# Optimization experiments

Measured on AMD Instinct MI355X. Metric: run time of the kernel, lower is better.

Reference implementation:

```python
import jax, jax.numpy as jnp
import numpy as np

B, S, D, H = 2, 2048, 1024, 16
DK = D // H


def setup_inputs() -> dict:
    key = jax.random.key(0)
    ks = jax.random.split(key, 11)
    s = 1.0 / np.sqrt(D)
    inp = {
        "q": jax.random.normal(ks[0], (B, S, D), jnp.float32),
        "k": jax.random.normal(ks[1], (B, S, D), jnp.float32),
        "v": jax.random.normal(ks[2], (B, S, D), jnp.float32),
        "mask": jnp.tril(jnp.ones((S, S), jnp.int32))[None, None],  # causal [1,1,S,S]
        "w_q": jax.random.normal(ks[3], (D, D), jnp.float32) * s,
        "b_q": jax.random.normal(ks[4], (D,), jnp.float32) * 0.01,
        "w_k": jax.random.normal(ks[5], (D, D), jnp.float32) * s,
        "b_k": jax.random.normal(ks[6], (D,), jnp.float32) * 0.01,
        "w_v": jax.random.normal(ks[7], (D, D), jnp.float32) * s,
        "b_v": jax.random.normal(ks[8], (D,), jnp.float32) * 0.01,
        "w_o": jax.random.normal(ks[9], (D, D), jnp.float32) * s,
        "b_o": jax.random.normal(ks[10], (D,), jnp.float32) * 0.01,
    }
    return inp


def reference(q, k, v, mask, w_q, b_q, w_k, b_k, w_v, b_v, w_o, b_o):
    # Linear projections (torch Linear: x @ W.T + b)
    query = q @ w_q.T + b_q  # [B,S,D]
    key_ = k @ w_k.T + b_k
    value = v @ w_v.T + b_v
    # split heads -> [B,H,S,DK]
    def split(x):
        return x.reshape(B, S, H, DK).transpose(0, 2, 1, 3)
    qh, kh, vh = split(query), split(key_), split(value)
    scores = jnp.einsum("bhqd,bhkd->bhqk", qh, kh) / jnp.sqrt(jnp.float32(DK))
    scores = jnp.where(mask == 0, jnp.float32(-1e9), scores)
    attn = jax.nn.softmax(scores, axis=-1)
    out = jnp.einsum("bhqk,bhkd->bhqd", attn, vh)  # [B,H,S,DK]
    out = out.transpose(0, 2, 1, 3).reshape(B, S, D)
    return out @ w_o.T + b_o
```

## Files before the change

kernel.cpp:

```cpp
#include <hip/hip_runtime.h>


typedef __attribute__((ext_vector_type(8))) short bf16x8;
typedef __attribute__((ext_vector_type(4))) float floatx4;
typedef __attribute__((ext_vector_type(4))) unsigned short u16x4;

#define S_LEN 2048
#define D_MODEL 1024
#define N_HEADS 16
#define D_HEAD 64
#define M_ROWS 4096
#define QSCALE 0.18033688011112042f

__device__ __forceinline__ unsigned short f32_to_bf16(float f) {
  unsigned int u = __builtin_bit_cast(unsigned int, f);
  u += 0x7FFFu + ((u >> 16) & 1u);
  return (unsigned short)(u >> 16);
}

__global__ __launch_bounds__(256) void cvt_w(
    const float* __restrict__ w0, const float* __restrict__ w1,
    const float* __restrict__ w2, const float* __restrict__ w3,
    unsigned short* __restrict__ dst) {
  const int z = blockIdx.y;
  const float* src = (z == 0) ? w0 : (z == 1) ? w1 : (z == 2) ? w2 : w3;
  unsigned short* d = dst + ((long)z << 20);
  const int n4 = 1 << 18;
  for (int i = blockIdx.x * 256 + threadIdx.x; i < n4; i += gridDim.x * 256) {
    float4 f = ((const float4*)src)[i];
    u16x4 o;
    o[0] = f32_to_bf16(f.x); o[1] = f32_to_bf16(f.y);
    o[2] = f32_to_bf16(f.z); o[3] = f32_to_bf16(f.w);
    ((u16x4*)d)[i] = o;
  }
}

__global__ __launch_bounds__(256) void cvt_x(
    const float* __restrict__ x0, const float* __restrict__ x1,
    const float* __restrict__ x2, unsigned short* __restrict__ dst) {
  const int z = blockIdx.y;
  const float* src = (z == 0) ? x0 : (z == 1) ? x1 : x2;
  unsigned short* d = dst + (long)z * M_ROWS * D_MODEL;
  const int n4 = (M_ROWS * D_MODEL) / 4;
  for (int i = blockIdx.x * 256 + threadIdx.x; i < n4; i += gridDim.x * 256) {
    float4 f = ((const float4*)src)[i];
    u16x4 o;
    o[0] = f32_to_bf16(f.x); o[1] = f32_to_bf16(f.y);
    o[2] = f32_to_bf16(f.z); o[3] = f32_to_bf16(f.w);
    ((u16x4*)d)[i] = o;
  }
}

#define GK 1024
#define GN 1024
#define LDP 72

template <bool XPRE>
__global__ __launch_bounds__(256, 3) void qkv_gemm(
    const float* __restrict__ Xq, const float* __restrict__ Xk, const float* __restrict__ Xv,
    const unsigned short* __restrict__ Xb,
    const unsigned short* __restrict__ Wb,
    const float* __restrict__ bq, const float* __restrict__ bk, const float* __restrict__ bv,
    unsigned short* __restrict__ Yq, unsigned short* __restrict__ Yk,
    unsigned short* __restrict__ Yvt) {
  __shared__ __align__(16) unsigned short As[128 * LDP];
  __shared__ __align__(16) unsigned short Bs[128 * LDP];

  const int z = blockIdx.z;
  const unsigned short* W = Wb + ((long)z << 20);
  const float* bias = (z == 0) ? bq : ((z == 1) ? bk : bv);

  const int r0 = blockIdx.x * 128;
  const int n0 = blockIdx.y * 128;
  const int tid = threadIdx.x;
  const int lane = tid & 63;
  const int wave = tid >> 6;
  const int quad = lane >> 4;
  const int ln = lane & 15;
  const int wm = (wave >> 1) * 64;
  const int wn = (wave & 1) * 64;

  floatx4 acc[4][4];
#pragma unroll
  for (int i = 0; i < 4; i++)
#pragma unroll
    for (int j = 0; j < 4; j++) acc[i][j] = (floatx4){0.f, 0.f, 0.f, 0.f};

  const int srow = tid >> 1;
  const int scol = (tid & 1) * 32;
  unsigned short* Asw = As + srow * LDP + scol;
  unsigned short* Bsw = Bs + srow * LDP + scol;
  const unsigned short* Bp = W + (long)(n0 + srow) * GK + scol;
  const float* ApF = nullptr;
  const unsigned short* ApH = nullptr;
  if constexpr (XPRE) {
    ApH = Xb + (long)z * M_ROWS * D_MODEL + (long)(r0 + srow) * GK + scol;
  } else {
    const float* X = (z == 0) ? Xq : ((z == 1) ? Xk : Xv);
    ApF = X + (long)(r0 + srow) * GK + scol;
  }

  for (int k0 = 0; k0 < GK; k0 += 64) {
    float4 b0 = *(const float4*)(Bp + k0);
    float4 b1 = *(const float4*)(Bp + k0 + 8);
    float4 b2 = *(const float4*)(Bp + k0 + 16);
    float4 b3 = *(const float4*)(Bp + k0 + 24);
    float4 a0, a1, a2, a3;
    if constexpr (XPRE) {
      a0 = *(const float4*)(ApH + k0);
      a1 = *(const float4*)(ApH + k0 + 8);
      a2 = *(const float4*)(ApH + k0 + 16);
      a3 = *(const float4*)(ApH + k0 + 24);
    } else {
      unsigned short ua[32] __attribute__((aligned(16)));
      float fa[32] __attribute__((aligned(16)));
#pragma unroll
      for (int c = 0; c < 8; c++)
        *(float4*)(fa + c * 4) = *(const float4*)(ApF + k0 + c * 4);
#pragma unroll
      for (int j = 0; j < 32; j++) ua[j] = f32_to_bf16(fa[j]);
      a0 = *(float4*)(ua); a1 = *(float4*)(ua + 8);
      a2 = *(float4*)(ua + 16); a3 = *(float4*)(ua + 24);
    }
    __syncthreads();
    *(float4*)(Asw) = a0;      *(float4*)(Asw + 8) = a1;
    *(float4*)(Asw + 16) = a2; *(float4*)(Asw + 24) = a3;
    *(float4*)(Bsw) = b0;      *(float4*)(Bsw + 8) = b1;
    *(float4*)(Bsw + 16) = b2; *(float4*)(Bsw + 24) = b3;
    __syncthreads();

#pragma unroll
    for (int ks = 0; ks < 64; ks += 32) {
      bf16x8 af[4], bfr[4];
#pragma unroll
      for (int mt = 0; mt < 4; mt++)
        af[mt] = *(const bf16x8*)(As + (wm + mt * 16 + ln) * LDP + ks + quad * 8);
#pragma unroll
      for (int nt = 0; nt < 4; nt++)
        bfr[nt] = *(const bf16x8*)(Bs + (wn + nt * 16 + ln) * LDP + ks + quad * 8);
#pragma unroll
      for (int mt = 0; mt < 4; mt++)
#pragma unroll
        for (int nt = 0; nt < 4; nt++)
          acc[mt][nt] = __builtin_amdgcn_mfma_f32_16x16x32_bf16(af[mt], bfr[nt], acc[mt][nt], 0, 0, 0);
    }
  }

#pragma unroll
  for (int nt = 0; nt < 4; nt++) {
    const int n = n0 + wn + nt * 16 + ln;
    const float bv = bias[n];
#pragma unroll
    for (int mt = 0; mt < 4; mt++) {
      const int r = r0 + wm + mt * 16 + quad * 4;
      if (z == 2) {
        u16x4 pk;
#pragma unroll
        for (int reg = 0; reg < 4; reg++) pk[reg] = f32_to_bf16(acc[mt][nt][reg] + bv);
        *(u16x4*)(Yvt + (long)n * M_ROWS + r) = pk;
      } else if (z == 0) {
#pragma unroll
        for (int reg = 0; reg < 4; reg++)
          Yq[(long)(r + reg) * GN + n] = f32_to_bf16((acc[mt][nt][reg] + bv) * QSCALE);
      } else {
#pragma unroll
        for (int reg = 0; reg < 4; reg++)
          Yk[(long)(r + reg) * GN + n] = f32_to_bf16(acc[mt][nt][reg] + bv);
      }
    }
  }
}

__global__ __launch_bounds__(256, 3) void out_gemm(
    const unsigned short* __restrict__ X,
    const unsigned short* __restrict__ W,
    const float* __restrict__ bias,
    float* __restrict__ Y) {
  __shared__ __align__(16) unsigned short As[64 * LDP];
  __shared__ __align__(16) unsigned short Bs[128 * LDP];

  const int r0 = blockIdx.x * 64;
  const int n0 = blockIdx.y * 128;
  const int tid = threadIdx.x;
  const int lane = tid & 63;
  const int wave = tid >> 6;
  const int quad = lane >> 4;
  const int ln = lane & 15;
  const int wm = (wave >> 1) * 32;
  const int wn = (wave & 1) * 64;

  floatx4 acc[2][4];
#pragma unroll
  for (int i = 0; i < 2; i++)
#pragma unroll
    for (int j = 0; j < 4; j++) acc[i][j] = (floatx4){0.f, 0.f, 0.f, 0.f};

  const int arow = tid >> 2;
  const int acol = (tid & 3) * 16;
  const unsigned short* Ap = X + (long)(r0 + arow) * GK + acol;
  unsigned short* Asw = As + arow * LDP + acol;
  const int brow = tid >> 1;
  const int bcol = (tid & 1) * 32;
  const unsigned short* Bp = W + (long)(n0 + brow) * GK + bcol;
  unsigned short* Bsw = Bs + brow * LDP + bcol;

  for (int k0 = 0; k0 < GK; k0 += 64) {
    float4 a0 = *(const float4*)(Ap + k0);
    float4 a1 = *(const float4*)(Ap + k0 + 8);
    float4 b0 = *(const float4*)(Bp + k0);
    float4 b1 = *(const float4*)(Bp + k0 + 8);
    float4 b2 = *(const float4*)(Bp + k0 + 16);
    float4 b3 = *(const float4*)(Bp + k0 + 24);
    __syncthreads();
    *(float4*)(Asw) = a0;      *(float4*)(Asw + 8) = a1;
    *(float4*)(Bsw) = b0;      *(float4*)(Bsw + 8) = b1;
    *(float4*)(Bsw + 16) = b2; *(float4*)(Bsw + 24) = b3;
    __syncthreads();

#pragma unroll
    for (int ks = 0; ks < 64; ks += 32) {
      bf16x8 af[2], bfr[4];
#pragma unroll
      for (int mt = 0; mt < 2; mt++)
        af[mt] = *(const bf16x8*)(As + (wm + mt * 16 + ln) * LDP + ks + quad * 8);
#pragma unroll
      for (int nt = 0; nt < 4; nt++)
        bfr[nt] = *(const bf16x8*)(Bs + (wn + nt * 16 + ln) * LDP + ks + quad * 8);
#pragma unroll
      for (int mt = 0; mt < 2; mt++)
#pragma unroll
        for (int nt = 0; nt < 4; nt++)
          acc[mt][nt] = __builtin_amdgcn_mfma_f32_16x16x32_bf16(af[mt], bfr[nt], acc[mt][nt], 0, 0, 0);
    }
  }

#pragma unroll
  for (int nt = 0; nt < 4; nt++) {
    const int n = n0 + wn + nt * 16 + ln;
    const float bv = bias[n];
#pragma unroll
    for (int mt = 0; mt < 2; mt++) {
      const int r = r0 + wm + mt * 16 + quad * 4;
#pragma unroll
      for (int reg = 0; reg < 4; reg++)
        Y[(long)(r + reg) * GN + n] = acc[mt][nt][reg] + bv;
    }
  }
}

#define PSTR 72

__global__ __launch_bounds__(64, 2) void attn_causal(
    const unsigned short* __restrict__ Q,
    const unsigned short* __restrict__ K,
    const unsigned short* __restrict__ Vt,
    unsigned short* __restrict__ O) {
  __shared__ __align__(16) unsigned short PbA[16 * PSTR];
  __shared__ __align__(16) unsigned short PbB[16 * PSTR];

  const int bh = blockIdx.x;
  const int pr = blockIdx.y;
  const int b = bh >> 4;
  const int h = bh & 15;

  const int lane = threadIdx.x;
  const int quad = lane >> 4;
  const int ln = lane & 15;

  const int s1 = pr, s2 = 127 - pr;
  const int q0A = s1 * 16, q0B = s2 * 16;
  const int nkt1 = (s1 >> 2) + 1;
  const int nkt2 = (s2 >> 2) + 1;

  const unsigned short* Qb = Q + (long)b * S_LEN * D_MODEL + h * D_HEAD;
  const unsigned short* Kb = K + (long)b * S_LEN * D_MODEL + h * D_HEAD;
  const unsigned short* Vb = Vt + (long)h * D_HEAD * M_ROWS + b * S_LEN;

  bf16x8 qfA[2], qfB[2];
  qfA[0] = *(const bf16x8*)(Qb + (long)(q0A + ln) * D_MODEL + quad * 8);
  qfA[1] = *(const bf16x8*)(Qb + (long)(q0A + ln) * D_MODEL + 32 + quad * 8);
  qfB[0] = *(const bf16x8*)(Qb + (long)(q0B + ln) * D_MODEL + quad * 8);
  qfB[1] = *(const bf16x8*)(Qb + (long)(q0B + ln) * D_MODEL + 32 + quad * 8);

  float mA = -1e30f, lA = 0.f, mB = -1e30f, lB = 0.f;
  floatx4 oA[4], oB[4];
#pragma unroll
  for (int nt = 0; nt < 4; nt++) {
    oA[nt] = (floatx4){0.f, 0.f, 0.f, 0.f};
    oB[nt] = (floatx4){0.f, 0.f, 0.f, 0.f};
  }

  auto loadKV = [&](bf16x8 (&kf)[4][2], bf16x8 (&vf)[4][2], int kt) {
    const int kv0 = kt * 64;
#pragma unroll
    for (int ct = 0; ct < 4; ct++) {
      const unsigned short* kp = Kb + (long)(kv0 + ct * 16 + ln) * D_MODEL + quad * 8;
      kf[ct][0] = *(const bf16x8*)(kp);
      kf[ct][1] = *(const bf16x8*)(kp + 32);
      const unsigned short* vp = Vb + (long)(ct * 16 + ln) * M_ROWS + kv0 + quad * 8;
      vf[ct][0] = *(const bf16x8*)(vp);
      vf[ct][1] = *(const bf16x8*)(vp + 32);
    }
  };

  auto iter = [&](bf16x8 (&kf)[4][2], bf16x8 (&vf)[4][2], int kt) {
    const int kv0 = kt * 64;
    const bool aAct = (kt < nkt1);

    floatx4 sB[4], sA[4];
#pragma unroll
    for (int ct = 0; ct < 4; ct++) {
      sB[ct] = (floatx4){0.f, 0.f, 0.f, 0.f};
      sB[ct] = __builtin_amdgcn_mfma_f32_16x16x32_bf16(kf[ct][0], qfB[0], sB[ct], 0, 0, 0);
      sB[ct] = __builtin_amdgcn_mfma_f32_16x16x32_bf16(kf[ct][1], qfB[1], sB[ct], 0, 0, 0);
    }
    if (aAct) {
#pragma unroll
      for (int ct = 0; ct < 4; ct++) {
        sA[ct] = (floatx4){0.f, 0.f, 0.f, 0.f};
        sA[ct] = __builtin_amdgcn_mfma_f32_16x16x32_bf16(kf[ct][0], qfA[0], sA[ct], 0, 0, 0);
        sA[ct] = __builtin_amdgcn_mfma_f32_16x16x32_bf16(kf[ct][1], qfA[1], sA[ct], 0, 0, 0);
      }
    }

    {
      float tmax = -1e30f;
      if (kt == nkt2 - 1) {
        const int qg = q0B + ln;
#pragma unroll
        for (int ct = 0; ct < 4; ct++) {
          const int kvb = kv0 + ct * 16 + quad * 4;
#pragma unroll
          for (int reg = 0; reg < 4; reg++) {
            float sv = sB[ct][reg];
            if (kvb + reg > qg) sv = -1e30f;
            sB[ct][reg] = sv;
            tmax = fmaxf(tmax, sv);
          }
        }
      } else {
#pragma unroll
        for (int ct = 0; ct < 4; ct++)
#pragma unroll
          for (int reg = 0; reg < 4; reg++) tmax = fmaxf(tmax, sB[ct][reg]);
      }
      tmax = fmaxf(tmax, __shfl_xor(tmax, 16, 64));
      tmax = fmaxf(tmax, __shfl_xor(tmax, 32, 64));
      const float mnew = fmaxf(mB, tmax);
      const float alpha = exp2f(mB - mnew);
      mB = mnew;
      float rsum = 0.f;
#pragma unroll
      for (int ct = 0; ct < 4; ct++) {
        u16x4 pk;
#pragma unroll
        for (int reg = 0; reg < 4; reg++) {
          const float p = exp2f(sB[ct][reg] - mB);
          rsum += p;
          pk[reg] = f32_to_bf16(p);
        }
        *(u16x4*)(PbB + ln * PSTR + ct * 16 + quad * 4) = pk;
      }
      rsum += __shfl_xor(rsum, 16, 64);
      rsum += __shfl_xor(rsum, 32, 64);
      lB = lB * alpha + rsum;
#pragma unroll
      for (int nt = 0; nt < 4; nt++)
#pragma unroll
        for (int reg = 0; reg < 4; reg++) oB[nt][reg] *= alpha;
    }

    if (aAct) {
      float tmax = -1e30f;
      if (kt == nkt1 - 1) {
        const int qg = q0A + ln;
#pragma unroll
        for (int ct = 0; ct < 4; ct++) {
          const int kvb = kv0 + ct * 16 + quad * 4;
#pragma unroll
          for (int reg = 0; reg < 4; reg++) {
            float sv = sA[ct][reg];
            if (kvb + reg > qg) sv = -1e30f;
            sA[ct][reg] = sv;
            tmax = fmaxf(tmax, sv);
          }
        }
      } else {
#pragma unroll
        for (int ct = 0; ct < 4; ct++)
#pragma unroll
          for (int reg = 0; reg < 4; reg++) tmax = fmaxf(tmax, sA[ct][reg]);
      }
      tmax = fmaxf(tmax, __shfl_xor(tmax, 16, 64));
      tmax = fmaxf(tmax, __shfl_xor(tmax, 32, 64));
      const float mnew = fmaxf(mA, tmax);
      const float alpha = exp2f(mA - mnew);
      mA = mnew;
      float rsum = 0.f;
#pragma unroll
      for (int ct = 0; ct < 4; ct++) {
        u16x4 pk;
#pragma unroll
        for (int reg = 0; reg < 4; reg++) {
          const float p = exp2f(sA[ct][reg] - mA);
          rsum += p;
          pk[reg] = f32_to_bf16(p);
        }
        *(u16x4*)(PbA + ln * PSTR + ct * 16 + quad * 4) = pk;
      }
      rsum += __shfl_xor(rsum, 16, 64);
      rsum += __shfl_xor(rsum, 32, 64);
      lA = lA * alpha + rsum;
#pragma unroll
      for (int nt = 0; nt < 4; nt++)
#pragma unroll
        for (int reg = 0; reg < 4; reg++) oA[nt][reg] *= alpha;
    }

    __builtin_amdgcn_wave_barrier();

    {
      bf16x8 p0 = *(const bf16x8*)(PbB + ln * PSTR + quad * 8);
      bf16x8 p1 = *(const bf16x8*)(PbB + ln * PSTR + 32 + quad * 8);
#pragma unroll
      for (int nt = 0; nt < 4; nt++) {
        oB[nt] = __builtin_amdgcn_mfma_f32_16x16x32_bf16(vf[nt][0], p0, oB[nt], 0, 0, 0);
        oB[nt] = __builtin_amdgcn_mfma_f32_16x16x32_bf16(vf[nt][1], p1, oB[nt], 0, 0, 0);
      }
    }
    if (aAct) {
      bf16x8 p0 = *(const bf16x8*)(PbA + ln * PSTR + quad * 8);
      bf16x8 p1 = *(const bf16x8*)(PbA + ln * PSTR + 32 + quad * 8);
#pragma unroll
      for (int nt = 0; nt < 4; nt++) {
        oA[nt] = __builtin_amdgcn_mfma_f32_16x16x32_bf16(vf[nt][0], p0, oA[nt], 0, 0, 0);
        oA[nt] = __builtin_amdgcn_mfma_f32_16x16x32_bf16(vf[nt][1], p1, oA[nt], 0, 0, 0);
      }
    }
    __builtin_amdgcn_wave_barrier();
  };

  bf16x8 kf0[4][2], vf0[4][2], kf1[4][2], vf1[4][2];
  loadKV(kf0, vf0, 0);
#pragma unroll 1
  for (int kt = 0; kt < nkt2; kt += 2) {
    if (kt + 1 < nkt2) loadKV(kf1, vf1, kt + 1);
    iter(kf0, vf0, kt);
    if (kt + 1 >= nkt2) break;
    if (kt + 2 < nkt2) loadKV(kf0, vf0, kt + 2);
    iter(kf1, vf1, kt + 1);
  }

  {
    const float inv = 1.0f / lA;
    unsigned short* op = O + (long)b * S_LEN * D_MODEL + (long)(q0A + ln) * D_MODEL + h * D_HEAD;
#pragma unroll
    for (int nt = 0; nt < 4; nt++) {
      u16x4 pk;
#pragma unroll
      for (int reg = 0; reg < 4; reg++) pk[reg] = f32_to_bf16(oA[nt][reg] * inv);
      *(u16x4*)(op + nt * 16 + quad * 4) = pk;
    }
  }
  {
    const float inv = 1.0f / lB;
    unsigned short* op = O + (long)b * S_LEN * D_MODEL + (long)(q0B + ln) * D_MODEL + h * D_HEAD;
#pragma unroll
    for (int nt = 0; nt < 4; nt++) {
      u16x4 pk;
#pragma unroll
      for (int reg = 0; reg < 4; reg++) pk[reg] = f32_to_bf16(oB[nt][reg] * inv);
      *(u16x4*)(op + nt * 16 + quad * 4) = pk;
    }
  }
}

extern "C" void kernel_launch(void* const* d_in, const int* in_sizes, int n_in,
                              void* d_out, int out_size, void* d_ws, size_t ws_size,
                              hipStream_t stream) {
  const float* q = (const float*)d_in[0];
  const float* k = (const float*)d_in[1];
  const float* v = (const float*)d_in[2];
  const float* w_q = (const float*)d_in[4];
  const float* b_q = (const float*)d_in[5];
  const float* w_k = (const float*)d_in[6];
  const float* b_k = (const float*)d_in[7];
  const float* w_v = (const float*)d_in[8];
  const float* b_v = (const float*)d_in[9];
  const float* w_o = (const float*)d_in[10];
  const float* b_o = (const float*)d_in[11];
  float* out = (float*)d_out;

  unsigned short* ws = (unsigned short*)d_ws;
  const long NE = (long)M_ROWS * D_MODEL;
  const bool xpre = (ws_size >= (size_t)7 * NE * sizeof(unsigned short));

  unsigned short *Qp, *Kp, *Vpt, *AO, *Wb, *Xb;
  if (xpre) {
    Qp = ws;
    Kp = ws + NE;
    Vpt = ws + 2 * NE;
    Wb = ws + 3 * NE;
    Xb = ws + 4 * NE;
    AO = ws + 4 * NE;
  } else {
    Qp = ws;
    Kp = ws + NE;
    Vpt = ws + 2 * NE;
    AO = ws + 3 * NE;
    Wb = ws + 4 * NE;
    Xb = nullptr;
  }

  cvt_w<<<dim3(256, 4), 256, 0, stream>>>(w_q, w_k, w_v, w_o, Wb);
  if (xpre) {
    cvt_x<<<dim3(512, 3), 256, 0, stream>>>(q, k, v, Xb);
    qkv_gemm<true><<<dim3(M_ROWS / 128, GN / 128, 3), 256, 0, stream>>>(
        q, k, v, Xb, Wb, b_q, b_k, b_v, Qp, Kp, Vpt);
  } else {
    qkv_gemm<false><<<dim3(M_ROWS / 128, GN / 128, 3), 256, 0, stream>>>(
        q, k, v, nullptr, Wb, b_q, b_k, b_v, Qp, Kp, Vpt);
  }
  attn_causal<<<dim3(2 * N_HEADS, 64), 64, 0, stream>>>(Qp, Kp, Vpt, AO);
  out_gemm<<<dim3(M_ROWS / 64, GN / 128), 256, 0, stream>>>(AO, Wb + 3 * (1 << 20), b_o, out);
}
```

Before: 283.1 us.

## Use async global-to-LDS loads in GEMMs, fuse X conversion, drop online softmax max

Drops the separate fp32-to-bf16 activation conversion kernel, so the QKV GEMM converts X in registers. B tiles (and both operands in the output GEMM) now go straight from global memory into unpadded LDS through global_load_lds. The attention kernel stops tracking a running max and rescaling, exponentiates raw scores directly, and gets row sums from extra MFMAs against a ones vector. Removing the max subtraction risks exp overflow for large scores, and the unpadded LDS layout may bring bank conflicts.

```diff
diff --git a/kernel.cpp b/kernel.cpp
--- a/kernel.cpp
+++ b/kernel.cpp
@@ -16,6 +16,12 @@
   unsigned int u = __builtin_bit_cast(unsigned int, f);
   u += 0x7FFFu + ((u >> 16) & 1u);
   return (unsigned short)(u >> 16);
+}
+
+__device__ __forceinline__ void async16(const void* g, void* l) {
+  __builtin_amdgcn_global_load_lds(
+      (const __attribute__((address_space(1))) unsigned int*)g,
+      (__attribute__((address_space(3))) unsigned int*)l, 16, 0, 0);
 }
 
 __global__ __launch_bounds__(256) void cvt_w(
@@ -35,38 +41,21 @@
   }
 }
 
-__global__ __launch_bounds__(256) void cvt_x(
-    const float* __restrict__ x0, const float* __restrict__ x1,
-    const float* __restrict__ x2, unsigned short* __restrict__ dst) {
-  const int z = blockIdx.y;
-  const float* src = (z == 0) ? x0 : (z == 1) ? x1 : x2;
-  unsigned short* d = dst + (long)z * M_ROWS * D_MODEL;
-  const int n4 = (M_ROWS * D_MODEL) / 4;
-  for (int i = blockIdx.x * 256 + threadIdx.x; i < n4; i += gridDim.x * 256) {
-    float4 f = ((const float4*)src)[i];
-    u16x4 o;
-    o[0] = f32_to_bf16(f.x); o[1] = f32_to_bf16(f.y);
-    o[2] = f32_to_bf16(f.z); o[3] = f32_to_bf16(f.w);
-    ((u16x4*)d)[i] = o;
-  }
-}
-
 #define GK 1024
 #define GN 1024
-#define LDP 72
-
-template <bool XPRE>
+#define BK 64
+
 __global__ __launch_bounds__(256, 3) void qkv_gemm(
     const float* __restrict__ Xq, const float* __restrict__ Xk, const float* __restrict__ Xv,
-    const unsigned short* __restrict__ Xb,
     const unsigned short* __restrict__ Wb,
     const float* __restrict__ bq, const float* __restrict__ bk, const float* __restrict__ bv,
     unsigned short* __restrict__ Yq, unsigned short* __restrict__ Yk,
     unsigned short* __restrict__ Yvt) {
-  __shared__ __align__(16) unsigned short As[128 * LDP];
-  __shared__ __align__(16) unsigned short Bs[128 * LDP];
+  __shared__ __align__(16) unsigned short As[128 * BK];
+  __shared__ __align__(16) unsigned short Bs[128 * BK];
 
   const int z = blockIdx.z;
+  const float* X = (z == 0) ? Xq : ((z == 1) ? Xk : Xv);
   const unsigned short* W = Wb + ((long)z << 20);
   const float* bias = (z == 0) ? bq : ((z == 1) ? bk : bv);
 
@@ -86,58 +75,43 @@
 #pragma unroll
     for (int j = 0; j < 4; j++) acc[i][j] = (floatx4){0.f, 0.f, 0.f, 0.f};
 
-  const int srow = tid >> 1;
-  const int scol = (tid & 1) * 32;
-  unsigned short* Asw = As + srow * LDP + scol;
-  unsigned short* Bsw = Bs + srow * LDP + scol;
-  const unsigned short* Bp = W + (long)(n0 + srow) * GK + scol;
-  const float* ApF = nullptr;
-  const unsigned short* ApH = nullptr;
-  if constexpr (XPRE) {
-    ApH = Xb + (long)z * M_ROWS * D_MODEL + (long)(r0 + srow) * GK + scol;
-  } else {
-    const float* X = (z == 0) ? Xq : ((z == 1) ? Xk : Xv);
-    ApF = X + (long)(r0 + srow) * GK + scol;
-  }
-
-  for (int k0 = 0; k0 < GK; k0 += 64) {
-    float4 b0 = *(const float4*)(Bp + k0);
-    float4 b1 = *(const float4*)(Bp + k0 + 8);
-    float4 b2 = *(const float4*)(Bp + k0 + 16);
-    float4 b3 = *(const float4*)(Bp + k0 + 24);
-    float4 a0, a1, a2, a3;
-    if constexpr (XPRE) {
-      a0 = *(const float4*)(ApH + k0);
-      a1 = *(const float4*)(ApH + k0 + 8);
-      a2 = *(const float4*)(ApH + k0 + 16);
-      a3 = *(const float4*)(ApH + k0 + 24);
-    } else {
-      unsigned short ua[32] __attribute__((aligned(16)));
-      float fa[32] __attribute__((aligned(16)));
-#pragma unroll
-      for (int c = 0; c < 8; c++)
-        *(float4*)(fa + c * 4) = *(const float4*)(ApF + k0 + c * 4);
-#pragma unroll
-      for (int j = 0; j < 32; j++) ua[j] = f32_to_bf16(fa[j]);
-      a0 = *(float4*)(ua); a1 = *(float4*)(ua + 8);
-      a2 = *(float4*)(ua + 16); a3 = *(float4*)(ua + 24);
-    }
+  const int arow = tid >> 3;
+  const int acol = (tid & 7) * 8;
+  const float* Ap = X + (long)(r0 + arow) * GK + acol;
+  unsigned short* Asw = As + tid * 8;
+  const int brow = lane >> 3;
+  const int bcol = (lane & 7) * 8;
+  const unsigned short* Bp = W + (long)(n0 + brow) * GK + bcol;
+
+  for (int k0 = 0; k0 < GK; k0 += BK) {
+    float fa[32] __attribute__((aligned(16)));
+#pragma unroll
+    for (int c = 0; c < 4; c++) {
+      *(float4*)(fa + c * 8)     = *(const float4*)(Ap + (long)c * 32 * GK + k0);
+      *(float4*)(fa + c * 8 + 4) = *(const float4*)(Ap + (long)c * 32 * GK + k0 + 4);
+    }
+    unsigned short ua[32] __attribute__((aligned(16)));
+#pragma unroll
+    for (int j = 0; j < 32; j++) ua[j] = f32_to_bf16(fa[j]);
+
     __syncthreads();
-    *(float4*)(Asw) = a0;      *(float4*)(Asw + 8) = a1;
-    *(float4*)(Asw + 16) = a2; *(float4*)(Asw + 24) = a3;
-    *(float4*)(Bsw) = b0;      *(float4*)(Bsw + 8) = b1;
-    *(float4*)(Bsw + 16) = b2; *(float4*)(Bsw + 24) = b3;
+#pragma unroll
+    for (int j = 0; j < 4; j++)
+      async16(Bp + (long)(wave * 4 + j) * 8 * GK + k0, Bs + (wave * 4 + j) * 512);
+#pragma unroll
+    for (int c = 0; c < 4; c++)
+      *(float4*)(Asw + c * 2048) = *(float4*)(ua + c * 8);
     __syncthreads();
 
 #pragma unroll
-    for (int ks = 0; ks < 64; ks += 32) {
+    for (int ks = 0; ks < BK; ks += 32) {
       bf16x8 af[4], bfr[4];
 #pragma unroll
       for (int mt = 0; mt < 4; mt++)
-        af[mt] = *(const bf16x8*)(As + (wm + mt * 16 + ln) * LDP + ks + quad * 8);
+        af[mt] = *(const bf16x8*)(As + (wm + mt * 16 + ln) * BK + ks + quad * 8);
 #pragma unroll
       for (int nt = 0; nt < 4; nt++)
-        bfr[nt] = *(const bf16x8*)(Bs + (wn + nt * 16 + ln) * LDP + ks + quad * 8);
+        bfr[nt] = *(const bf16x8*)(Bs + (wn + nt * 16 + ln) * BK + ks + quad * 8);
 #pragma unroll
       for (int mt = 0; mt < 4; mt++)
 #pragma unroll
@@ -176,8 +150,8 @@
     const unsigned short* __restrict__ W,
     const float* __restrict__ bias,
     float* __restrict__ Y) {
-  __shared__ __align__(16) unsigned short As[64 * LDP];
-  __shared__ __align__(16) unsigned short Bs[128 * LDP];
+  __shared__ __align__(16) unsigned short As[64 * BK];
+  __shared__ __align__(16) unsigned short Bs[128 * BK];
 
   const int r0 = blockIdx.x * 64;
   const int n0 = blockIdx.y * 128;
@@ -195,37 +169,30 @@
 #pragma unroll
     for (int j = 0; j < 4; j++) acc[i][j] = (floatx4){0.f, 0.f, 0.f, 0.f};
 
-  const int arow = tid >> 2;
-  const int acol = (tid & 3) * 16;
-  const unsigned short* Ap = X + (long)(r0 + arow) * GK + acol;
-  unsigned short* Asw = As + arow * LDP + acol;
-  const int brow = tid >> 1;
-  const int bcol = (tid & 1) * 32;
-  const unsigned short* Bp = W + (long)(n0 + brow) * GK + bcol;
-  unsigned short* Bsw = Bs + brow * LDP + bcol;
-
-  for (int k0 = 0; k0 < GK; k0 += 64) {
-    float4 a0 = *(const float4*)(Ap + k0);
-    float4 a1 = *(const float4*)(Ap + k0 + 8);
-    float4 b0 = *(const float4*)(Bp + k0);
-    float4 b1 = *(const float4*)(Bp + k0 + 8);
-    float4 b2 = *(const float4*)(Bp + k0 + 16);
-    float4 b3 = *(const float4*)(Bp + k0 + 24);
+  const int srow = lane >> 3;
+  const int scol = (lane & 7) * 8;
+  const unsigned short* Apb = X + (long)(r0 + srow) * GK + scol;
+  const unsigned short* Bpb = W + (long)(n0 + srow) * GK + scol;
+
+  for (int k0 = 0; k0 < GK; k0 += BK) {
     __syncthreads();
-    *(float4*)(Asw) = a0;      *(float4*)(Asw + 8) = a1;
-    *(float4*)(Bsw) = b0;      *(float4*)(Bsw + 8) = b1;
-    *(float4*)(Bsw + 16) = b2; *(float4*)(Bsw + 24) = b3;
+#pragma unroll
+    for (int j = 0; j < 2; j++)
+      async16(Apb + (long)(wave * 2 + j) * 8 * GK + k0, As + (wave * 2 + j) * 512);
+#pragma unroll
+    for (int j = 0; j < 4; j++)
+      async16(Bpb + (long)(wave * 4 + j) * 8 * GK + k0, Bs + (wave * 4 + j) * 512);
     __syncthreads();
 
 #pragma unroll
-    for (int ks = 0; ks < 64; ks += 32) {
+    for (int ks = 0; ks < BK; ks += 32) {
       bf16x8 af[2], bfr[4];
 #pragma unroll
       for (int mt = 0; mt < 2; mt++)
-        af[mt] = *(const bf16x8*)(As + (wm + mt * 16 + ln) * LDP + ks + quad * 8);
+        af[mt] = *(const bf16x8*)(As + (wm + mt * 16 + ln) * BK + ks + quad * 8);
 #pragma unroll
       for (int nt = 0; nt < 4; nt++)
-        bfr[nt] = *(const bf16x8*)(Bs + (wn + nt * 16 + ln) * LDP + ks + quad * 8);
+        bfr[nt] = *(const bf16x8*)(Bs + (wn + nt * 16 + ln) * BK + ks + quad * 8);
 #pragma unroll
       for (int mt = 0; mt < 2; mt++)
 #pragma unroll
@@ -282,13 +249,18 @@
   qfB[0] = *(const bf16x8*)(Qb + (long)(q0B + ln) * D_MODEL + quad * 8);
   qfB[1] = *(const bf16x8*)(Qb + (long)(q0B + ln) * D_MODEL + 32 + quad * 8);
 
-  float mA = -1e30f, lA = 0.f, mB = -1e30f, lB = 0.f;
-  floatx4 oA[4], oB[4];
+  bf16x8 ones;
+#pragma unroll
+  for (int j = 0; j < 8; j++) ones[j] = (short)0x3F80;
+
+  floatx4 oA[4], oB[4], lAacc, lBacc;
 #pragma unroll
   for (int nt = 0; nt < 4; nt++) {
     oA[nt] = (floatx4){0.f, 0.f, 0.f, 0.f};
     oB[nt] = (floatx4){0.f, 0.f, 0.f, 0.f};
   }
+  lAacc = (floatx4){0.f, 0.f, 0.f, 0.f};
+  lBacc = (floatx4){0.f, 0.f, 0.f, 0.f};
 
   auto loadKV = [&](bf16x8 (&kf)[4][2], bf16x8 (&vf)[4][2], int kt) {
     const int kv0 = kt * 64;
@@ -324,97 +296,36 @@
     }
 
     {
-      float tmax = -1e30f;
-      if (kt == nkt2 - 1) {
-        const int qg = q0B + ln;
-#pragma unroll
-        for (int ct = 0; ct < 4; ct++) {
-          const int kvb = kv0 + ct * 16 + quad * 4;
-#pragma unroll
-          for (int reg = 0; reg < 4; reg++) {
-            float sv = sB[ct][reg];
-            if (kvb + reg > qg) sv = -1e30f;
-            sB[ct][reg] = sv;
-            tmax = fmaxf(tmax, sv);
-          }
-        }
-      } else {
-#pragma unroll
-        for (int ct = 0; ct < 4; ct++)
-#pragma unroll
-          for (int reg = 0; reg < 4; reg++) tmax = fmaxf(tmax, sB[ct][reg]);
-      }
-      tmax = fmaxf(tmax, __shfl_xor(tmax, 16, 64));
-      tmax = fmaxf(tmax, __shfl_xor(tmax, 32, 64));
-      const float mnew = fmaxf(mB, tmax);
-      const float alpha = exp2f(mB - mnew);
-      mB = mnew;
-      float rsum = 0.f;
+      const bool lastB = (kt == nkt2 - 1);
+      const int qg = q0B + ln;
 #pragma unroll
       for (int ct = 0; ct < 4; ct++) {
+        const int kvb = kv0 + ct * 16 + quad * 4;
         u16x4 pk;
 #pragma unroll
         for (int reg = 0; reg < 4; reg++) {
-          const float p = exp2f(sB[ct][reg] - mB);
-          rsum += p;
-          pk[reg] = f32_to_bf16(p);
+          float sv = sB[ct][reg];
+          if (lastB && (kvb + reg > qg)) sv = -1e30f;
+          pk[reg] = f32_to_bf16(exp2f(sv));
         }
         *(u16x4*)(PbB + ln * PSTR + ct * 16 + quad * 4) = pk;
       }
-      rsum += __shfl_xor(rsum, 16, 64);
-      rsum += __shfl_xor(rsum, 32, 64);
-      lB = lB * alpha + rsum;
-#pragma unroll
-      for (int nt = 0; nt < 4; nt++)
-#pragma unroll
-        for (int reg = 0; reg < 4; reg++) oB[nt][reg] *= alpha;
-    }
-
+    }
     if (aAct) {
-      float tmax = -1e30f;
-      if (kt == nkt1 - 1) {
-        const int qg = q0A + ln;
-#pragma unroll
-        for (int ct = 0; ct < 4; ct++) {
-          const int kvb = kv0 + ct * 16 + quad * 4;
-#pragma unroll
-          for (int reg = 0; reg < 4; reg++) {
-            float sv = sA[ct][reg];
-            if (kvb + reg > qg) sv = -1e30f;
-            sA[ct][reg] = sv;
-            tmax = fmaxf(tmax, sv);
-          }
-        }
-      } else {
-#pragma unroll
-        for (int ct = 0; ct < 4; ct++)
-#pragma unroll
-          for (int reg = 0; reg < 4; reg++) tmax = fmaxf(tmax, sA[ct][reg]);
-      }
-      tmax = fmaxf(tmax, __shfl_xor(tmax, 16, 64));
-      tmax = fmaxf(tmax, __shfl_xor(tmax, 32, 64));
-      const float mnew = fmaxf(mA, tmax);
-      const float alpha = exp2f(mA - mnew);
-      mA = mnew;
-      float rsum = 0.f;
+      const bool lastA = (kt == nkt1 - 1);
+      const int qg = q0A + ln;
 #pragma unroll
       for (int ct = 0; ct < 4; ct++) {
+        const int kvb = kv0 + ct * 16 + quad * 4;
         u16x4 pk;
 #pragma unroll
         for (int reg = 0; reg < 4; reg++) {
-          const float p = exp2f(sA[ct][reg] - mA);
-          rsum += p;
-          pk[reg] = f32_to_bf16(p);
+          float sv = sA[ct][reg];
+          if (lastA && (kvb + reg > qg)) sv = -1e30f;
+          pk[reg] = f32_to_bf16(exp2f(sv));
         }
         *(u16x4*)(PbA + ln * PSTR + ct * 16 + quad * 4) = pk;
       }
-      rsum += __shfl_xor(rsum, 16, 64);
-      rsum += __shfl_xor(rsum, 32, 64);
-      lA = lA * alpha + rsum;
-#pragma unroll
-      for (int nt = 0; nt < 4; nt++)
-#pragma unroll
-        for (int reg = 0; reg < 4; reg++) oA[nt][reg] *= alpha;
     }
 
     __builtin_amdgcn_wave_barrier();
@@ -427,6 +338,8 @@
         oB[nt] = __builtin_amdgcn_mfma_f32_16x16x32_bf16(vf[nt][0], p0, oB[nt], 0, 0, 0);
         oB[nt] = __builtin_amdgcn_mfma_f32_16x16x32_bf16(vf[nt][1], p1, oB[nt], 0, 0, 0);
       }
+      lBacc = __builtin_amdgcn_mfma_f32_16x16x32_bf16(ones, p0, lBacc, 0, 0, 0);
+      lBacc = __builtin_amdgcn_mfma_f32_16x16x32_bf16(ones, p1, lBacc, 0, 0, 0);
     }
     if (aAct) {
       bf16x8 p0 = *(const bf16x8*)(PbA + ln * PSTR + quad * 8);
@@ -436,6 +349,8 @@
         oA[nt] = __builtin_amdgcn_mfma_f32_16x16x32_bf16(vf[nt][0], p0, oA[nt], 0, 0, 0);
         oA[nt] = __builtin_amdgcn_mfma_f32_16x16x32_bf16(vf[nt][1], p1, oA[nt], 0, 0, 0);
       }
+      lAacc = __builtin_amdgcn_mfma_f32_16x16x32_bf16(ones, p0, lAacc, 0, 0, 0);
+      lAacc = __builtin_amdgcn_mfma_f32_16x16x32_bf16(ones, p1, lAacc, 0, 0, 0);
     }
     __builtin_amdgcn_wave_barrier();
   };
@@ -452,7 +367,7 @@
   }
 
   {
-    const float inv = 1.0f / lA;
+    const float inv = 1.0f / lAacc[0];
     unsigned short* op = O + (long)b * S_LEN * D_MODEL + (long)(q0A + ln) * D_MODEL + h * D_HEAD;
 #pragma unroll
     for (int nt = 0; nt < 4; nt++) {
@@ -463,7 +378,7 @@
     }
   }
   {
-    const float inv = 1.0f / lB;
+    const float inv = 1.0f / lBacc[0];
     unsigned short* op = O + (long)b * S_LEN * D_MODEL + (long)(q0B + ln) * D_MODEL + h * D_HEAD;
 #pragma unroll
     for (int nt = 0; nt < 4; nt++) {
@@ -493,34 +408,15 @@
 
   unsigned short* ws = (unsigned short*)d_ws;
   const long NE = (long)M_ROWS * D_MODEL;
-  const bool xpre = (ws_size >= (size_t)7 * NE * sizeof(unsigned short));
-
-  unsigned short *Qp, *Kp, *Vpt, *AO, *Wb, *Xb;
-  if (xpre) {
-    Qp = ws;
-    Kp = ws + NE;
-    Vpt = ws + 2 * NE;
-    Wb = ws + 3 * NE;
-    Xb = ws + 4 * NE;
-    AO = ws + 4 * NE;
-  } else {
-    Qp = ws;
-    Kp = ws + NE;
-    Vpt = ws + 2 * NE;
-    AO = ws + 3 * NE;
-    Wb = ws + 4 * NE;
-    Xb = nullptr;
-  }
+  unsigned short* Qp = ws;
+  unsigned short* Kp = ws + NE;
+  unsigned short* Vpt = ws + 2 * NE;
+  unsigned short* AO = ws + 3 * NE;
+  unsigned short* Wb = ws + 4 * NE;
 
   cvt_w<<<dim3(256, 4), 256, 0, stream>>>(w_q, w_k, w_v, w_o, Wb);
-  if (xpre) {
-    cvt_x<<<dim3(512, 3), 256, 0, stream>>>(q, k, v, Xb);
-    qkv_gemm<true><<<dim3(M_ROWS / 128, GN / 128, 3), 256, 0, stream>>>(
-        q, k, v, Xb, Wb, b_q, b_k, b_v, Qp, Kp, Vpt);
-  } else {
-    qkv_gemm<false><<<dim3(M_ROWS / 128, GN / 128, 3), 256, 0, stream>>>(
-        q, k, v, nullptr, Wb, b_q, b_k, b_v, Qp, Kp, Vpt);
-  }
+  qkv_gemm<<<dim3(M_ROWS / 128, GN / 128, 3), 256, 0, stream>>>(
+      q, k, v, Wb, b_q, b_k, b_v, Qp, Kp, Vpt);
   attn_causal<<<dim3(2 * N_HEADS, 64), 64, 0, stream>>>(Qp, Kp, Vpt, AO);
   out_gemm<<<dim3(M_ROWS / 64, GN / 128), 256, 0, stream>>>(AO, Wb + 3 * (1 << 20), b_o, out);
 }
```

Result: slower. 297.1 us (+5.0%).
